# Performance work log

Measured on AMD Instinct MI355X. Metric: run time of the kernel, lower is better.

## Reference

```python
import jax, jax.numpy as jnp
import numpy as np

B, N, D_IN = 4, 2048, 1024
H, D_OUT = 8, 128


def setup_inputs() -> dict:
    key = jax.random.key(0)
    k1, k2, k3 = jax.random.split(key, 3)
    x = jax.random.normal(k1, (B, N, D_IN), dtype=jnp.float32)
    # W: (num_head, 3 [q,k,v], d_in, output_dim), glorot-ish scale
    W = jax.random.normal(k2, (H, 3, D_IN, D_OUT), dtype=jnp.float32) * (1.0 / np.sqrt(D_IN))
    Wo = jax.random.normal(k3, (H * D_OUT, D_OUT), dtype=jnp.float32) * (1.0 / np.sqrt(H * D_OUT))
    return {"x": x, "W": W, "Wo": Wo}


def reference(x, W, Wo):
    # Per-head QKV projections, vectorized over heads.
    # q,k,v: [B, H, N, D_OUT]
    q = jnp.einsum("bnd,hde->bhne", x, W[:, 0])
    k = jnp.einsum("bnd,hde->bhne", x, W[:, 1])
    v = jnp.einsum("bnd,hde->bhne", x, W[:, 2])
    scale = 1.0 / jnp.sqrt(jnp.asarray(D_OUT, dtype=x.dtype))
    # scores: [B, H, N, N]
    e = jnp.einsum("bhne,bhme->bhnm", q, k) * scale
    a = jax.nn.softmax(e, axis=-1)
    o = jnp.einsum("bhnm,bhme->bhne", a, v)  # [B, H, N, D_OUT]
    # concat heads -> [B, N, H*D_OUT]; head i occupies slice [i*D_OUT:(i+1)*D_OUT]
    o = jnp.transpose(o, (0, 2, 1, 3)).reshape(x.shape[0], x.shape[1], H * D_OUT)
    z = jnp.einsum("bnf,fe->bne", o, Wo)  # [B, N, D_OUT]
    return z
```

## Files before the change

### kernel.cpp

```cpp
#include <hip/hip_runtime.h>
#include <cstdint>


#define DEV __device__ __forceinline__

typedef _Float16 h8 __attribute__((ext_vector_type(8)));
typedef _Float16 h4 __attribute__((ext_vector_type(4)));
typedef float f4 __attribute__((ext_vector_type(4)));

typedef __attribute__((address_space(1))) const uint32_t gu32;
typedef __attribute__((address_space(3))) uint32_t lu32;

DEV float fexp2(float x) { return __builtin_amdgcn_exp2f(x); }

DEV f4 mfma16(h8 a, h8 b, f4 c) {
  return __builtin_amdgcn_mfma_f32_16x16x32_f16(a, b, c, 0, 0, 0);
}

DEV void g2l16(void* lds, const void* g) {
  __builtin_amdgcn_global_load_lds((gu32*)(uintptr_t)g, (lu32*)(uintptr_t)lds,
                                   16, 0, 0);
}

DEV f4 sx4(f4 v, int m) {
  f4 r;
  r[0] = __shfl_xor(v[0], m, 64);
  r[1] = __shfl_xor(v[1], m, 64);
  r[2] = __shfl_xor(v[2], m, 64);
  r[3] = __shfl_xor(v[3], m, 64);
  return r;
}

__global__ __launch_bounds__(256) void cvt_x_kernel(const float* __restrict__ x,
                                                    _Float16* __restrict__ Xb) {
  size_t i = (size_t)(blockIdx.x * 256 + threadIdx.x) * 4;
  f4 v = *(const f4*)(x + i);
  h4 o;
  o[0] = (_Float16)v[0];
  o[1] = (_Float16)v[1];
  o[2] = (_Float16)v[2];
  o[3] = (_Float16)v[3];
  *(h4*)(Xb + i) = o;
}

__global__ __launch_bounds__(256) void cvt_wt_kernel(const float* __restrict__ W,
                                                     const float* __restrict__ Wo,
                                                     _Float16* __restrict__ WT,
                                                     _Float16* __restrict__ WoT) {
  __shared__ float st[64][68];
  const int mz = blockIdx.z;
  const float* src = (mz < 24) ? (W + (size_t)mz * 131072) : Wo;
  _Float16* dst = (mz < 24) ? (WT + (size_t)mz * 131072) : WoT;
  const int d0 = blockIdx.x * 64;
  const int e0 = blockIdx.y * 64;
  const int tid = threadIdx.x;
#pragma unroll
  for (int r = 0; r < 4; ++r) {
    int idx = r * 256 + tid;
    int dd = idx >> 4, cc = (idx & 15) * 4;
    f4 v = *(const f4*)(src + (size_t)(d0 + dd) * 128 + e0 + cc);
    *(f4*)&st[dd][cc] = v;
  }
  __syncthreads();
#pragma unroll
  for (int r = 0; r < 2; ++r) {
    int idx = r * 256 + tid;
    int ee = idx >> 3, dd = (idx & 7) * 8;
    h8 o;
#pragma unroll
    for (int i = 0; i < 8; ++i) o[i] = (_Float16)st[dd + i][ee];
    *(h8*)(dst + (size_t)(e0 + ee) * 1024 + d0 + dd) = o;
  }
}

template <int MODE>
__global__ __launch_bounds__(256, 2) void gemm_bt_kernel(
    const _Float16* __restrict__ A, const _Float16* __restrict__ BTall,
    _Float16* __restrict__ Qb, _Float16* __restrict__ Kb,
    _Float16* __restrict__ VTb, float* __restrict__ outF) {
  constexpr int K = 1024;
  __shared__ __align__(16) _Float16 sAB[16384];
  const int tid = threadIdx.x;
  const int wave = tid >> 6, lane = tid & 63;
  const int g = lane >> 4, l15 = lane & 15;
  const int sw = l15 & 7;
  const int m0 = blockIdx.x * 128;
  const int j = blockIdx.y;
  const _Float16* BT = BTall + (size_t)j * (128 * 1024);

  f4 acc[4][4] = {};
  const int ar = (wave >> 1) * 64 + l15;
  const int br = (wave & 1) * 64 + l15;

#pragma unroll 1
  for (int kt = 0; kt < K; kt += 64) {
    __syncthreads();
#pragma unroll
    for (int r = 0; r < 4; ++r) {
      int idx = r * 256 + tid;
      int row = idx >> 3;
      int jg = (idx & 7) ^ (row & 7);
      g2l16(&sAB[idx * 8], A + (size_t)(m0 + row) * K + kt + jg * 8);
      g2l16(&sAB[8192 + idx * 8], BT + (size_t)row * K + kt + jg * 8);
    }
    __syncthreads();
#pragma unroll
    for (int ks = 0; ks < 2; ++ks) {
      int off = ((ks * 4 + g) ^ sw) * 8;
      h8 af[4], bf[4];
#pragma unroll
      for (int mt = 0; mt < 4; ++mt)
        af[mt] = *(const h8*)&sAB[(ar + mt * 16) * 64 + off];
#pragma unroll
      for (int nt = 0; nt < 4; ++nt)
        bf[nt] = *(const h8*)&sAB[8192 + (br + nt * 16) * 64 + off];
#pragma unroll
      for (int mt = 0; mt < 4; ++mt)
#pragma unroll
        for (int nt = 0; nt < 4; ++nt)
          acc[mt][nt] = mfma16(af[mt], bf[nt], acc[mt][nt]);
    }
  }

  const int wr = (wave >> 1) * 64, wc = (wave & 1) * 64;
  if (MODE == 0) {
    const int h = j / 3, s = j - h * 3;
    if (s < 2) {
      const float scl = (s == 0) ? 0.12751741032075984f : 1.0f;
      _Float16* dst = (s == 0) ? Qb : Kb;
      __syncthreads();
#pragma unroll
      for (int mt = 0; mt < 4; ++mt)
#pragma unroll
        for (int rg = 0; rg < 4; ++rg) {
          int rl = wr + mt * 16 + g * 4 + rg;
#pragma unroll
          for (int nt = 0; nt < 4; ++nt) {
            int c = wc + nt * 16 + l15;
            sAB[rl * 128 + (((c >> 3) ^ (rl & 7)) * 8) + (c & 7)] =
                (_Float16)(acc[mt][nt][rg] * scl);
          }
        }
      __syncthreads();
      int rr = tid >> 1, seg = tid & 1;
      int m = m0 + rr, b = m >> 11, n = m & 2047;
      size_t rb = ((size_t)((b * 8 + h) * 2048 + n)) * 128;
#pragma unroll
      for (int k = 0; k < 8; ++k) {
        int ch = seg * 8 + k;
        h8 v = *(const h8*)&sAB[rr * 128 + ((ch ^ (rr & 7)) * 8)];
        *(h8*)&dst[rb + ch * 8] = v;
      }
    } else {
      __syncthreads();
      const int b = m0 >> 11, n0 = m0 & 2047;
      size_t base = (size_t)(b * 8 + h) * (128 * 2048);
#pragma unroll
      for (int mt = 0; mt < 4; ++mt)
#pragma unroll
        for (int rg = 0; rg < 4; ++rg) {
          int nl = wr + mt * 16 + g * 4 + rg;
          int cc = (nl >> 3), ci = nl & 7;
#pragma unroll
          for (int nt = 0; nt < 4; ++nt) {
            int c = wc + nt * 16 + l15;
            sAB[c * 128 + ((cc ^ (c & 7)) * 8) + ci] = (_Float16)acc[mt][nt][rg];
          }
        }
      __syncthreads();
      int c = tid >> 1, seg = tid & 1;
#pragma unroll
      for (int k = 0; k < 8; ++k) {
        int ch = seg * 8 + k;
        h8 v = *(const h8*)&sAB[c * 128 + ((ch ^ (c & 7)) * 8)];
        *(h8*)&VTb[base + (size_t)c * 2048 + n0 + ch * 8] = v;
      }
    }
  } else {
#pragma unroll
    for (int mt = 0; mt < 4; ++mt)
#pragma unroll
      for (int rg = 0; rg < 4; ++rg) {
        int m = m0 + wr + mt * 16 + g * 4 + rg;
#pragma unroll
        for (int nt = 0; nt < 4; ++nt)
          outF[(size_t)m * 128 + wc + nt * 16 + l15] = acc[mt][nt][rg];
      }
  }
}

__global__ __launch_bounds__(256, 3) void flash_kernel(
    const _Float16* __restrict__ Qb, const _Float16* __restrict__ Kb,
    const _Float16* __restrict__ VTb, _Float16* __restrict__ Oc) {
  __shared__ __align__(16) _Float16 sK[64 * 128];
  __shared__ __align__(16) _Float16 sVT[128 * 64];
  __shared__ __align__(16) _Float16 sP[4 * 32 * 64];
  const int tid = threadIdx.x, wave = tid >> 6, lane = tid & 63;
  const int g = lane >> 4, l15 = lane & 15;
  const int sw = l15 & 7;
  const int bh = blockIdx.x, b = bh >> 3, h = bh & 7;
  const int q0 = blockIdx.y * 128;
  const _Float16* Q = Qb + (size_t)bh * (2048 * 128);
  const _Float16* Kp = Kb + (size_t)bh * (2048 * 128);
  const _Float16* VT = VTb + (size_t)bh * (128 * 2048);
  _Float16* sPw = &sP[wave * (32 * 64)];

  h8 qf[2][4];
#pragma unroll
  for (int mt = 0; mt < 2; ++mt)
#pragma unroll
    for (int kk = 0; kk < 4; ++kk)
      qf[mt][kk] = *(const h8*)&Q[(size_t)(q0 + wave * 32 + mt * 16 + l15) * 128 +
                                  kk * 32 + g * 8];

  f4 oacc[2][8] = {};
  f4 lstate[2] = {};

#pragma unroll 1
  for (int kv0 = 0; kv0 < 2048; kv0 += 64) {
    __syncthreads();
#pragma unroll
    for (int r = 0; r < 4; ++r) {
      int idx = r * 256 + tid;
      int row = idx >> 4;
      int jg = (idx & 15) ^ (row & 7);
      g2l16(&sK[idx * 8], Kp + (size_t)(kv0 + row) * 128 + jg * 8);
      int row2 = idx >> 3;
      int jg2 = (idx & 7) ^ (row2 & 7);
      g2l16(&sVT[idx * 8], VT + (size_t)row2 * 2048 + kv0 + jg2 * 8);
    }
    __syncthreads();

    f4 sacc[2][4] = {};
#pragma unroll
    for (int kk = 0; kk < 4; ++kk) {
      int off = ((kk * 4 + g) ^ sw) * 8;
#pragma unroll
      for (int nt = 0; nt < 4; ++nt) {
        h8 bf = *(const h8*)&sK[(nt * 16 + l15) * 128 + off];
        sacc[0][nt] = mfma16(qf[0][kk], bf, sacc[0][nt]);
        sacc[1][nt] = mfma16(qf[1][kk], bf, sacc[1][nt]);
      }
    }

#pragma unroll
    for (int mt = 0; mt < 2; ++mt) {
#pragma unroll
      for (int nt = 0; nt < 4; ++nt) {
        f4 p;
        p[0] = fexp2(sacc[mt][nt][0]);
        p[1] = fexp2(sacc[mt][nt][1]);
        p[2] = fexp2(sacc[mt][nt][2]);
        p[3] = fexp2(sacc[mt][nt][3]);
        lstate[mt] += p;
        int cc = nt * 2 + (l15 >> 3), ci = l15 & 7;
#pragma unroll
        for (int rg = 0; rg < 4; ++rg) {
          int rl = mt * 16 + g * 4 + rg;
          sPw[rl * 64 + ((cc ^ (rl & 7)) * 8) + ci] = (_Float16)p[rg];
        }
      }
    }

#pragma unroll
    for (int kk = 0; kk < 2; ++kk) {
      int off = ((kk * 4 + g) ^ sw) * 8;
      h8 pa0 = *(const h8*)&sPw[l15 * 64 + off];
      h8 pa1 = *(const h8*)&sPw[(16 + l15) * 64 + off];
#pragma unroll
      for (int nt = 0; nt < 8; ++nt) {
        h8 vb = *(const h8*)&sVT[(nt * 16 + l15) * 64 + off];
        oacc[0][nt] = mfma16(pa0, vb, oacc[0][nt]);
        oacc[1][nt] = mfma16(pa1, vb, oacc[1][nt]);
      }
    }
  }

#pragma unroll
  for (int mt = 0; mt < 2; ++mt) {
#pragma unroll
    for (int d = 1; d < 16; d <<= 1) lstate[mt] += sx4(lstate[mt], d);
    f4 inv;
    inv[0] = 1.0f / lstate[mt][0];
    inv[1] = 1.0f / lstate[mt][1];
    inv[2] = 1.0f / lstate[mt][2];
    inv[3] = 1.0f / lstate[mt][3];
#pragma unroll
    for (int rg = 0; rg < 4; ++rg) {
      int n = q0 + wave * 32 + mt * 16 + g * 4 + rg;
      size_t rb = ((size_t)(b * 2048 + n)) * 1024 + h * 128;
#pragma unroll
      for (int nt = 0; nt < 8; ++nt)
        Oc[rb + nt * 16 + l15] = (_Float16)(oacc[mt][nt][rg] * inv[rg]);
    }
  }
}

extern "C" void kernel_launch(void* const* d_in, const int* in_sizes, int n_in,
                              void* d_out, int out_size, void* d_ws,
                              size_t ws_size, hipStream_t stream) {
  const float* x = (const float*)d_in[0];
  const float* W = (const float*)d_in[1];
  const float* Wo = (const float*)d_in[2];
  float* out = (float*)d_out;
  char* ws = (char*)d_ws;

  _Float16* Xb = (_Float16*)(ws + 0);
  _Float16* WT = (_Float16*)(ws + 16777216);
  _Float16* WoT = (_Float16*)(ws + 23068672);
  _Float16* Qb = (_Float16*)(ws + 23330816);
  _Float16* Kb = (_Float16*)(ws + 40108032);
  _Float16* VTb = (_Float16*)(ws + 56885248);
  _Float16* Oc = (_Float16*)(ws + 73662464);

  cvt_x_kernel<<<8192, 256, 0, stream>>>(x, Xb);
  cvt_wt_kernel<<<dim3(16, 2, 25), 256, 0, stream>>>(W, Wo, WT, WoT);
  gemm_bt_kernel<0><<<dim3(64, 24), 256, 0, stream>>>(Xb, WT, Qb, Kb, VTb,
                                                      nullptr);
  flash_kernel<<<dim3(32, 16), 256, 0, stream>>>(Qb, Kb, VTb, Oc);
  gemm_bt_kernel<1><<<dim3(64, 1), 256, 0, stream>>>(Oc, WoT, nullptr, nullptr,
                                                     nullptr, out);
}
```

Baseline: 281.3 us.

## Split flash attention over KV halves and add combine and small-tile output GEMM

The flash kernel now splits the KV range into two halves along a new grid dimension, writes unnormalized partial outputs and row sums, and a new combine kernel sums the halves and normalizes. The output projection GEMM is replaced by a dedicated kernel with 32-row tiles, giving 256 blocks instead of 64. The P scratch buffer uses padded rows in place of the XOR swizzle. The aim is more parallelism on a GPU that was underfilled by 512 attention blocks and 64 GEMM blocks, at the cost of extra launches and extra partial-output memory traffic. The split works without max subtraction because scores are never max-shifted, and fp16 partials risk overflow.

```diff
diff --git a/kernel.cpp b/kernel.cpp
--- a/kernel.cpp
+++ b/kernel.cpp
@@ -73,11 +73,10 @@
   }
 }
 
-template <int MODE>
-__global__ __launch_bounds__(256, 2) void gemm_bt_kernel(
+__global__ __launch_bounds__(256, 2) void gemm_qkv_kernel(
     const _Float16* __restrict__ A, const _Float16* __restrict__ BTall,
     _Float16* __restrict__ Qb, _Float16* __restrict__ Kb,
-    _Float16* __restrict__ VTb, float* __restrict__ outF) {
+    _Float16* __restrict__ VTb) {
   constexpr int K = 1024;
   __shared__ __align__(16) _Float16 sAB[16384];
   const int tid = threadIdx.x;
@@ -123,87 +122,79 @@
   }
 
   const int wr = (wave >> 1) * 64, wc = (wave & 1) * 64;
-  if (MODE == 0) {
-    const int h = j / 3, s = j - h * 3;
-    if (s < 2) {
-      const float scl = (s == 0) ? 0.12751741032075984f : 1.0f;
-      _Float16* dst = (s == 0) ? Qb : Kb;
-      __syncthreads();
-#pragma unroll
-      for (int mt = 0; mt < 4; ++mt)
-#pragma unroll
-        for (int rg = 0; rg < 4; ++rg) {
-          int rl = wr + mt * 16 + g * 4 + rg;
-#pragma unroll
-          for (int nt = 0; nt < 4; ++nt) {
-            int c = wc + nt * 16 + l15;
-            sAB[rl * 128 + (((c >> 3) ^ (rl & 7)) * 8) + (c & 7)] =
-                (_Float16)(acc[mt][nt][rg] * scl);
-          }
+  const int h = j / 3, s = j - h * 3;
+  if (s < 2) {
+    const float scl = (s == 0) ? 0.12751741032075984f : 1.0f;
+    _Float16* dst = (s == 0) ? Qb : Kb;
+    __syncthreads();
+#pragma unroll
+    for (int mt = 0; mt < 4; ++mt)
+#pragma unroll
+      for (int rg = 0; rg < 4; ++rg) {
+        int rl = wr + mt * 16 + g * 4 + rg;
+#pragma unroll
+        for (int nt = 0; nt < 4; ++nt) {
+          int c = wc + nt * 16 + l15;
+          sAB[rl * 128 + (((c >> 3) ^ (rl & 7)) * 8) + (c & 7)] =
+              (_Float16)(acc[mt][nt][rg] * scl);
         }
-      __syncthreads();
-      int rr = tid >> 1, seg = tid & 1;
-      int m = m0 + rr, b = m >> 11, n = m & 2047;
-      size_t rb = ((size_t)((b * 8 + h) * 2048 + n)) * 128;
-#pragma unroll
-      for (int k = 0; k < 8; ++k) {
-        int ch = seg * 8 + k;
-        h8 v = *(const h8*)&sAB[rr * 128 + ((ch ^ (rr & 7)) * 8)];
-        *(h8*)&dst[rb + ch * 8] = v;
-      }
-    } else {
-      __syncthreads();
-      const int b = m0 >> 11, n0 = m0 & 2047;
-      size_t base = (size_t)(b * 8 + h) * (128 * 2048);
-#pragma unroll
-      for (int mt = 0; mt < 4; ++mt)
-#pragma unroll
-        for (int rg = 0; rg < 4; ++rg) {
-          int nl = wr + mt * 16 + g * 4 + rg;
-          int cc = (nl >> 3), ci = nl & 7;
-#pragma unroll
-          for (int nt = 0; nt < 4; ++nt) {
-            int c = wc + nt * 16 + l15;
-            sAB[c * 128 + ((cc ^ (c & 7)) * 8) + ci] = (_Float16)acc[mt][nt][rg];
-          }
+      }
+    __syncthreads();
+    int rr = tid >> 1, seg = tid & 1;
+    int m = m0 + rr, b = m >> 11, n = m & 2047;
+    size_t rb = ((size_t)((b * 8 + h) * 2048 + n)) * 128;
+#pragma unroll
+    for (int k = 0; k < 8; ++k) {
+      int ch = seg * 8 + k;
+      h8 v = *(const h8*)&sAB[rr * 128 + ((ch ^ (rr & 7)) * 8)];
+      *(h8*)&dst[rb + ch * 8] = v;
+    }
+  } else {
+    __syncthreads();
+    const int b = m0 >> 11, n0 = m0 & 2047;
+    size_t base = (size_t)(b * 8 + h) * (128 * 2048);
+#pragma unroll
+    for (int mt = 0; mt < 4; ++mt)
+#pragma unroll
+      for (int rg = 0; rg < 4; ++rg) {
+        int nl = wr + mt * 16 + g * 4 + rg;
+        int cc = (nl >> 3), ci = nl & 7;
+#pragma unroll
+        for (int nt = 0; nt < 4; ++nt) {
+          int c = wc + nt * 16 + l15;
+          sAB[c * 128 + ((cc ^ (c & 7)) * 8) + ci] = (_Float16)acc[mt][nt][rg];
         }
-      __syncthreads();
-      int c = tid >> 1, seg = tid & 1;
-#pragma unroll
-      for (int k = 0; k < 8; ++k) {
-        int ch = seg * 8 + k;
-        h8 v = *(const h8*)&sAB[c * 128 + ((ch ^ (c & 7)) * 8)];
-        *(h8*)&VTb[base + (size_t)c * 2048 + n0 + ch * 8] = v;
-      }
-    }
-  } else {
-#pragma unroll
-    for (int mt = 0; mt < 4; ++mt)
-#pragma unroll
-      for (int rg = 0; rg < 4; ++rg) {
-        int m = m0 + wr + mt * 16 + g * 4 + rg;
-#pragma unroll
-        for (int nt = 0; nt < 4; ++nt)
-          outF[(size_t)m * 128 + wc + nt * 16 + l15] = acc[mt][nt][rg];
-      }
+      }
+    __syncthreads();
+    int c = tid >> 1, seg = tid & 1;
+#pragma unroll
+    for (int k = 0; k < 8; ++k) {
+      int ch = seg * 8 + k;
+      h8 v = *(const h8*)&sAB[c * 128 + ((ch ^ (c & 7)) * 8)];
+      *(h8*)&VTb[base + (size_t)c * 2048 + n0 + ch * 8] = v;
+    }
   }
 }
 
 __global__ __launch_bounds__(256, 3) void flash_kernel(
     const _Float16* __restrict__ Qb, const _Float16* __restrict__ Kb,
-    const _Float16* __restrict__ VTb, _Float16* __restrict__ Oc) {
+    const _Float16* __restrict__ VTb, _Float16* __restrict__ O0,
+    _Float16* __restrict__ O1, float* __restrict__ Lpart) {
   __shared__ __align__(16) _Float16 sK[64 * 128];
   __shared__ __align__(16) _Float16 sVT[128 * 64];
-  __shared__ __align__(16) _Float16 sP[4 * 32 * 64];
+  __shared__ __align__(16) _Float16 sP[4 * 32 * 72];
   const int tid = threadIdx.x, wave = tid >> 6, lane = tid & 63;
   const int g = lane >> 4, l15 = lane & 15;
   const int sw = l15 & 7;
   const int bh = blockIdx.x, b = bh >> 3, h = bh & 7;
   const int q0 = blockIdx.y * 128;
+  const int kvbase = blockIdx.z * 1024;
   const _Float16* Q = Qb + (size_t)bh * (2048 * 128);
   const _Float16* Kp = Kb + (size_t)bh * (2048 * 128);
   const _Float16* VT = VTb + (size_t)bh * (128 * 2048);
-  _Float16* sPw = &sP[wave * (32 * 64)];
+  _Float16* Op = (blockIdx.z == 0) ? O0 : O1;
+  float* Lp = Lpart + (size_t)blockIdx.z * 65536;
+  _Float16* sPw = &sP[wave * (32 * 72)];
 
   h8 qf[2][4];
 #pragma unroll
@@ -217,7 +208,8 @@
   f4 lstate[2] = {};
 
 #pragma unroll 1
-  for (int kv0 = 0; kv0 < 2048; kv0 += 64) {
+  for (int t = 0; t < 16; ++t) {
+    const int kv0 = kvbase + t * 64;
     __syncthreads();
 #pragma unroll
     for (int r = 0; r < 4; ++r) {
@@ -244,7 +236,7 @@
     }
 
 #pragma unroll
-    for (int mt = 0; mt < 2; ++mt) {
+    for (int mt = 0; mt < 2; ++mt)
 #pragma unroll
       for (int nt = 0; nt < 4; ++nt) {
         f4 p;
@@ -253,20 +245,17 @@
         p[2] = fexp2(sacc[mt][nt][2]);
         p[3] = fexp2(sacc[mt][nt][3]);
         lstate[mt] += p;
-        int cc = nt * 2 + (l15 >> 3), ci = l15 & 7;
-#pragma unroll
-        for (int rg = 0; rg < 4; ++rg) {
-          int rl = mt * 16 + g * 4 + rg;
-          sPw[rl * 64 + ((cc ^ (rl & 7)) * 8) + ci] = (_Float16)p[rg];
-        }
-      }
-    }
-
-#pragma unroll
-    for (int kk = 0; kk < 2; ++kk) {
-      int off = ((kk * 4 + g) ^ sw) * 8;
-      h8 pa0 = *(const h8*)&sPw[l15 * 64 + off];
-      h8 pa1 = *(const h8*)&sPw[(16 + l15) * 64 + off];
+#pragma unroll
+        for (int rg = 0; rg < 4; ++rg)
+          sPw[(mt * 16 + g * 4 + rg) * 72 + nt * 16 + l15] = (_Float16)p[rg];
+      }
+
+#pragma unroll
+    for (int kk2 = 0; kk2 < 2; ++kk2) {
+      int po = kk2 * 32 + g * 8;
+      h8 pa0 = *(const h8*)&sPw[l15 * 72 + po];
+      h8 pa1 = *(const h8*)&sPw[(16 + l15) * 72 + po];
+      int off = ((kk2 * 4 + g) ^ sw) * 8;
 #pragma unroll
       for (int nt = 0; nt < 8; ++nt) {
         h8 vb = *(const h8*)&sVT[(nt * 16 + l15) * 64 + off];
@@ -280,20 +269,86 @@
   for (int mt = 0; mt < 2; ++mt) {
 #pragma unroll
     for (int d = 1; d < 16; d <<= 1) lstate[mt] += sx4(lstate[mt], d);
-    f4 inv;
-    inv[0] = 1.0f / lstate[mt][0];
-    inv[1] = 1.0f / lstate[mt][1];
-    inv[2] = 1.0f / lstate[mt][2];
-    inv[3] = 1.0f / lstate[mt][3];
 #pragma unroll
     for (int rg = 0; rg < 4; ++rg) {
       int n = q0 + wave * 32 + mt * 16 + g * 4 + rg;
       size_t rb = ((size_t)(b * 2048 + n)) * 1024 + h * 128;
 #pragma unroll
       for (int nt = 0; nt < 8; ++nt)
-        Oc[rb + nt * 16 + l15] = (_Float16)(oacc[mt][nt][rg] * inv[rg]);
-    }
-  }
+        Op[rb + nt * 16 + l15] = (_Float16)oacc[mt][nt][rg];
+      if (l15 == 0) Lp[(size_t)(b * 2048 + n) * 8 + h] = lstate[mt][rg];
+    }
+  }
+}
+
+__global__ __launch_bounds__(256) void combine_kernel(
+    const _Float16* __restrict__ O0, const _Float16* __restrict__ O1,
+    const float* __restrict__ L0, const float* __restrict__ L1,
+    _Float16* __restrict__ Oc) {
+  size_t i = (size_t)(blockIdx.x * 256 + threadIdx.x) * 8;
+  int lidx = (int)(i >> 7);
+  float inv = 1.0f / (L0[lidx] + L1[lidx]);
+  h8 a = *(const h8*)(O0 + i);
+  h8 c = *(const h8*)(O1 + i);
+  h8 o;
+#pragma unroll
+  for (int j = 0; j < 8; ++j)
+    o[j] = (_Float16)(((float)a[j] + (float)c[j]) * inv);
+  *(h8*)(Oc + i) = o;
+}
+
+__global__ __launch_bounds__(256, 2) void gemm_out_kernel(
+    const _Float16* __restrict__ A, const _Float16* __restrict__ BT,
+    float* __restrict__ outF) {
+  __shared__ __align__(16) _Float16 sA[32 * 64];
+  __shared__ __align__(16) _Float16 sB[128 * 64];
+  const int tid = threadIdx.x, wave = tid >> 6, lane = tid & 63;
+  const int g = lane >> 4, l15 = lane & 15, sw = l15 & 7;
+  const int m0 = blockIdx.x * 32;
+  f4 acc[2][2] = {};
+
+#pragma unroll 1
+  for (int kt = 0; kt < 1024; kt += 64) {
+    __syncthreads();
+    {
+      int row = tid >> 3;
+      int jg = (tid & 7) ^ (row & 7);
+      g2l16(&sA[tid * 8], A + (size_t)(m0 + row) * 1024 + kt + jg * 8);
+    }
+#pragma unroll
+    for (int r = 0; r < 4; ++r) {
+      int idx = r * 256 + tid;
+      int row = idx >> 3;
+      int jg = (idx & 7) ^ (row & 7);
+      g2l16(&sB[idx * 8], BT + (size_t)row * 1024 + kt + jg * 8);
+    }
+    __syncthreads();
+#pragma unroll
+    for (int ks = 0; ks < 2; ++ks) {
+      int off = ((ks * 4 + g) ^ sw) * 8;
+      h8 af[2], bf[2];
+#pragma unroll
+      for (int mt = 0; mt < 2; ++mt)
+        af[mt] = *(const h8*)&sA[(mt * 16 + l15) * 64 + off];
+#pragma unroll
+      for (int nt = 0; nt < 2; ++nt)
+        bf[nt] = *(const h8*)&sB[(wave * 32 + nt * 16 + l15) * 64 + off];
+#pragma unroll
+      for (int mt = 0; mt < 2; ++mt)
+#pragma unroll
+        for (int nt = 0; nt < 2; ++nt)
+          acc[mt][nt] = mfma16(af[mt], bf[nt], acc[mt][nt]);
+    }
+  }
+#pragma unroll
+  for (int mt = 0; mt < 2; ++mt)
+#pragma unroll
+    for (int rg = 0; rg < 4; ++rg) {
+      int m = m0 + mt * 16 + g * 4 + rg;
+#pragma unroll
+      for (int nt = 0; nt < 2; ++nt)
+        outF[(size_t)m * 128 + wave * 32 + nt * 16 + l15] = acc[mt][nt][rg];
+    }
 }
 
 extern "C" void kernel_launch(void* const* d_in, const int* in_sizes, int n_in,
@@ -312,12 +367,14 @@
   _Float16* Kb = (_Float16*)(ws + 40108032);
   _Float16* VTb = (_Float16*)(ws + 56885248);
   _Float16* Oc = (_Float16*)(ws + 73662464);
+  _Float16* O0 = Xb;
+  _Float16* O1 = (_Float16*)(ws + 90439680);
+  float* Lpart = (float*)(ws + 107216896);
 
   cvt_x_kernel<<<8192, 256, 0, stream>>>(x, Xb);
   cvt_wt_kernel<<<dim3(16, 2, 25), 256, 0, stream>>>(W, Wo, WT, WoT);
-  gemm_bt_kernel<0><<<dim3(64, 24), 256, 0, stream>>>(Xb, WT, Qb, Kb, VTb,
-                                                      nullptr);
-  flash_kernel<<<dim3(32, 16), 256, 0, stream>>>(Qb, Kb, VTb, Oc);
-  gemm_bt_kernel<1><<<dim3(64, 1), 256, 0, stream>>>(Oc, WoT, nullptr, nullptr,
-                                                     nullptr, out);
-}
+  gemm_qkv_kernel<<<dim3(64, 24), 256, 0, stream>>>(Xb, WT, Qb, Kb, VTb);
+  flash_kernel<<<dim3(32, 16, 2), 256, 0, stream>>>(Qb, Kb, VTb, O0, O1, Lpart);
+  combine_kernel<<<4096, 256, 0, stream>>>(O0, O1, Lpart, Lpart + 65536, Oc);
+  gemm_out_kernel<<<256, 256, 0, stream>>>(Oc, WoT, out);
+}
```

Result: slower. 293.0 us (+4.2%).
